# Performance work log

Hardware: AMD Instinct MI355X
Metric: run time of the kernel (lower is better)

## Reference

```python
import jax, jax.numpy as jnp
import numpy as np

HEADS = 8
DIM_HEAD = 64
QUERY_DIM = 320
INNER = HEADS * DIM_HEAD
B = 1
N = 2304          # 48*48 latent pixels
HS = WS = 48
SCALE = DIM_HEAD ** -0.5
ATTN_MATRIX_SCALE = 1.5   # injection_config['T']


def setup_inputs() -> dict:
    key = jax.random.key(0)
    ks = jax.random.split(key, 10)
    f = lambda k, s: jax.random.normal(k, s, dtype=jnp.float32)
    return {
        'x': f(ks[0], (B, N, QUERY_DIM)),
        'Wq': f(ks[1], (QUERY_DIM, INNER)) * 0.05,
        'Wo': f(ks[2], (INNER, QUERY_DIM)) * 0.05,
        'bo': jnp.zeros((QUERY_DIM,), jnp.float32),
        'q_injected': f(ks[3], (B * HEADS, N, DIM_HEAD)),
        'k_injected': f(ks[4], (B * HEADS, N, DIM_HEAD)),
        'v_injected': f(ks[5], (B * HEADS, N, DIM_HEAD)),
        'cnt_k_injected': f(ks[6], (B * HEADS, N, DIM_HEAD)),
        'cnt_v_injected': f(ks[7], (B * HEADS, N, DIM_HEAD)),
        'mask': jax.random.uniform(ks[8], (HS, WS), dtype=jnp.float32),
    }


def _split_heads(t):
    # 'b n (h d) -> (b h) n d'
    b, n, _ = t.shape
    return t.reshape(b, n, HEADS, DIM_HEAD).transpose(0, 2, 1, 3).reshape(b * HEADS, n, DIM_HEAD)


def reference(x, Wq, Wo, bo, q_injected, k_injected, v_injected,
              cnt_k_injected, cnt_v_injected, mask):
    # --- q/k/v with injection (b=1 so torch.cat([.]*b) is identity) ---
    q_in = q_injected                          # (bh, N, d)
    q_ = _split_heads(x @ Wq)                  # to_q(x) -> (bh, N, d)
    q = 0.5 * q_in + 0.5 * q_                  # blended query
    k = k_injected
    v = v_injected
    q_cnt, k_cnt, v_cnt = q_in, cnt_k_injected, cnt_v_injected

    # --- get_batch_sim: content-content similarity (b=1 => rearrange is identity) ---
    cc_sim = jnp.einsum('hid,hjd->hij', q_cnt, k_cnt) * SCALE     # (h, N, N)

    # --- get_batch_sim_with_mask ---
    sim = jnp.einsum('hid,hjd->hij', q, k) * (ATTN_MATRIX_SCALE * SCALE)  # (h, N, N)
    sim_r = sim.reshape(HEADS, HS, WS, N)
    cc_r = cc_sim.reshape(HEADS, HS, WS, N)
    max_sim = jnp.einsum('hid,hjd->hij', q_cnt, k)                # delta_q x delta_k (=self.k)
    max_sim_r = max_sim.reshape(HEADS, HS, WS, N)
    min_cc = jnp.min(cc_r, axis=3, keepdims=True)                 # (h, HS, WS, 1)
    max_ms = jnp.max(max_sim_r, axis=3, keepdims=True)            # (h, HS, WS, 1)

    # binary-threshold the mask, flip sign, bilinear-resize to (HS, WS)
    m = jnp.where(mask < 0.5, -1.0, jnp.where(mask > 0.5, 1.0, mask)) * -1.0
    m = jax.image.resize(m[None, None], (1, 1, HS, WS), method='bilinear')
    m = m.reshape(1, HS, WS, 1)

    gvm = (min_cc - max_ms) * m                                   # gradual_vanished_mask
    sim = (sim_r + gvm).reshape(HEADS, N, N)                      # rows [:WS] == all rows here

    # B=1 => the view/permute/reshape block is identity: sim, cc_sim are (h, N, N)
    # concatenated softmax over style keys and content keys
    cat_sim = jnp.concatenate([sim, cc_sim], axis=2)              # (h, N, 2N)
    cat_attn = jax.nn.softmax(cat_sim, axis=-1)
    cat_v = jnp.concatenate([v, v_cnt], axis=1)                   # (h, 2N, d)
    cat_out = jnp.einsum('hij,hjd->hid', cat_attn, cat_v)         # (h, N, d)

    # 'h (b n) d -> b n (h d)' with b=1
    out = cat_out.transpose(1, 0, 2).reshape(B, N, INNER)
    return out @ Wo + bo
```

## Files before the change

kernel.cpp:

```cpp
#include <hip/hip_runtime.h>
#include <math.h>

#define HEADS 8
#define NTOK  2304
#define DH    64
#define QD    320
#define INNER 512
#define TPS   36
#define PSTR  68

typedef _Float16 f16;
typedef f16  f16x4 __attribute__((ext_vector_type(4)));
typedef f16  f16x8 __attribute__((ext_vector_type(8)));
typedef float f32x4 __attribute__((ext_vector_type(4)));

#define MFMA(a,b,c) __builtin_amdgcn_mfma_f32_16x16x32_f16((a),(b),(c),0,0,0)

#define GLDS(gp, lp) __builtin_amdgcn_global_load_lds(                      \
    (const __attribute__((address_space(1))) void*)(gp),                    \
    (__attribute__((address_space(3))) void*)(lp), 16, 0, 0)

#if __has_builtin(__builtin_amdgcn_exp2f)
#define EXP2(x) __builtin_amdgcn_exp2f(x)
#else
#define EXP2(x) exp2f(x)
#endif

#define LOG2E 1.44269504f

static __device__ __forceinline__ unsigned pkrtz(float a, float b) {
#if __has_builtin(__builtin_amdgcn_cvt_pkrtz)
  return __builtin_bit_cast(unsigned, __builtin_amdgcn_cvt_pkrtz(a, b));
#else
  union { f16 h[2]; unsigned u; } c;
  c.h[0] = (f16)a; c.h[1] = (f16)b;
  return c.u;
#endif
}

__global__ __launch_bounds__(256) void prep_all(
    const float* __restrict__ qi, const float* __restrict__ ki,
    const float* __restrict__ kc, const float* __restrict__ x,
    const float* __restrict__ v,  const float* __restrict__ vc,
    const float* __restrict__ Wq, const float* __restrict__ Wo,
    f16* __restrict__ oq, f16* __restrict__ ok, f16* __restrict__ okc,
    f16* __restrict__ ox, f16* __restrict__ vt, f16* __restrict__ vct,
    f16* __restrict__ WqT, f16* __restrict__ WoT)
{
  __shared__ float T[64][65];
  const int bid = blockIdx.x;
  const int tid = threadIdx.x;

  if (bid < 2088) {
    int i = bid * 256 + tid;
    const float* src; f16* dst; float s = 1.0f; int off;
    if (i < 147456)      { src = qi; dst = oq;  off = i; }
    else if (i < 294912) { src = ki; dst = ok;  off = i - 147456; }
    else if (i < 442368) { src = kc; dst = okc; off = i - 294912; s = 0.125f * LOG2E; }
    else                 { src = x;  dst = ox;  off = i - 442368; }
    float4 a = reinterpret_cast<const float4*>(src)[off * 2];
    float4 b = reinterpret_cast<const float4*>(src)[off * 2 + 1];
    f16x8 o;
    o[0] = (f16)(a.x * s); o[1] = (f16)(a.y * s);
    o[2] = (f16)(a.z * s); o[3] = (f16)(a.w * s);
    o[4] = (f16)(b.x * s); o[5] = (f16)(b.y * s);
    o[6] = (f16)(b.z * s); o[7] = (f16)(b.w * s);
    *reinterpret_cast<f16x8*>(&dst[(size_t)off * 8]) = o;
  } else if (bid < 2664) {
    int t = bid - 2088;
    int z = t / 288, rem = t % 288;
    int h = rem / 36, nt = rem % 36;
    const float* src = z ? vc : v;
    f16* dst = z ? vct : vt;
    const int n0 = nt * 64;
    const size_t base = ((size_t)h * NTOK + n0) * DH;
    for (int it = 0; it < 4; ++it) {
      int idx = tid + it * 256;
      int n = idx >> 4, d0 = (idx & 15) * 4;
      float4 a = *reinterpret_cast<const float4*>(&src[base + (size_t)n * DH + d0]);
      T[n][d0] = a.x; T[n][d0 + 1] = a.y; T[n][d0 + 2] = a.z; T[n][d0 + 3] = a.w;
    }
    __syncthreads();
    for (int it = 0; it < 2; ++it) {
      int idx = tid + it * 256;
      int d = idx >> 3, c0 = (idx & 7) * 8;
      f16x8 o;
      #pragma unroll
      for (int i = 0; i < 8; ++i) o[i] = (f16)T[c0 + i][d];
      *reinterpret_cast<f16x8*>(&dst[(size_t)(h * 64 + d) * NTOK + n0 + c0]) = o;
    }
  } else {
    int t = bid - 2664;
    int z = t / 40, b = t % 40;
    const float* src = z ? Wo : Wq;
    f16* dst = z ? WoT : WqT;
    const int R = z ? INNER : QD;
    const int C = z ? QD : INNER;
    const int ctiles = C >> 6;
    const int rt = b / ctiles, ct = b % ctiles;
    for (int it = 0; it < 4; ++it) {
      int idx = tid + it * 256;
      int r = idx >> 4, c4 = (idx & 15) * 4;
      float4 a = *reinterpret_cast<const float4*>(&src[(size_t)(rt * 64 + r) * C + ct * 64 + c4]);
      T[r][c4] = a.x; T[r][c4 + 1] = a.y; T[r][c4 + 2] = a.z; T[r][c4 + 3] = a.w;
    }
    __syncthreads();
    for (int it = 0; it < 4; ++it) {
      int idx = tid + it * 256;
      int c = idx >> 4, r4 = (idx & 15) * 4;
      f16x4 o;
      #pragma unroll
      for (int i = 0; i < 4; ++i) o[i] = (f16)T[r4 + i][c];
      *reinterpret_cast<f16x4*>(&dst[(size_t)(ct * 64 + c) * R + rt * 64 + r4]) = o;
    }
  }
}

__global__ __launch_bounds__(256) void qblend_mfma(
    const f16* __restrict__ x16, const f16* __restrict__ WqT,
    const float* __restrict__ qinj, f16* __restrict__ qhat)
{
  const int qt = blockIdx.x, h = blockIdx.y;
  const int n0 = qt * 32;
  const int tid = threadIdx.x;
  const int w = tid >> 6, l = tid & 63, lq = l & 15, lk = l >> 4;
  const int qsub = w & 1, ch = w >> 1;
  f32x4 acc[2] = {};
  const f16* arow = x16 + (size_t)(n0 + qsub * 16 + lq) * QD;
  #pragma unroll
  for (int ks = 0; ks < 10; ++ks) {
    f16x8 a = *reinterpret_cast<const f16x8*>(&arow[ks * 32 + lk * 8]);
    #pragma unroll
    for (int df = 0; df < 2; ++df) {
      const f16* brow = WqT + (size_t)(h * 64 + ch * 32 + df * 16 + lq) * QD;
      f16x8 b = *reinterpret_cast<const f16x8*>(&brow[ks * 32 + lk * 8]);
      acc[df] = MFMA(a, b, acc[df]);
    }
  }
  const float sc = 0.09375f * LOG2E;
  #pragma unroll
  for (int df = 0; df < 2; ++df)
    #pragma unroll
    for (int r = 0; r < 4; ++r) {
      int n = n0 + qsub * 16 + lk * 4 + r;
      int d = ch * 32 + df * 16 + lq;
      size_t idx = ((size_t)h * NTOK + n) * DH + d;
      qhat[idx] = (f16)(sc * (qinj[idx] + acc[df][r]));
    }
}

__global__ __launch_bounds__(128, 2) void attn_nx(
    const f16* __restrict__ qhat, const f16* __restrict__ qc16,
    const f16* __restrict__ k16,  const f16* __restrict__ kc16,
    const f16* __restrict__ vt16, const f16* __restrict__ vct16,
    float* __restrict__ part)
{
  __shared__ __align__(16) f16 smem[2][2][2048];
  __shared__ __align__(16) f16 pbuf[2][640];

  const int bid = blockIdx.x;
  const int h    = bid & 7;
  const int strm = (bid >> 3) & 1;
  const int sp   = (bid >> 4) & 1;
  const int qt   = bid >> 5;
  const int tid = threadIdx.x;
  const int w = tid >> 6, l = tid & 63;
  const int lq = l & 15, lk = l >> 4;
  const size_t hb = (size_t)h * NTOK * DH;
  const int row0 = qt * 96 + w * 48 + lq;

  f16x8 qh0[2], qh1[2], qh2[2], qc0[2], qc1[2], qc2[2];
  {
    const size_t qr0 = hb + (size_t)row0 * DH;
    #pragma unroll
    for (int ks = 0; ks < 2; ++ks) {
      const int o = ks * 32 + lk * 8;
      qc0[ks] = *reinterpret_cast<const f16x8*>(&qc16[qr0 + o]);
      qc1[ks] = *reinterpret_cast<const f16x8*>(&qc16[qr0 + 16 * DH + o]);
      qc2[ks] = *reinterpret_cast<const f16x8*>(&qc16[qr0 + 32 * DH + o]);
      if (!strm) {
        qh0[ks] = *reinterpret_cast<const f16x8*>(&qhat[qr0 + o]);
        qh1[ks] = *reinterpret_cast<const f16x8*>(&qhat[qr0 + 16 * DH + o]);
        qh2[ks] = *reinterpret_cast<const f16x8*>(&qhat[qr0 + 32 * DH + o]);
      } else { qh0[ks] = qc0[ks]; qh1[ks] = qc1[ks]; qh2[ks] = qc2[ks]; }
    }
  }

  const int krow = tid >> 3;
  const int ksw  = ((tid & 7) ^ (krow & 7)) * 8;
  const int vrow = tid >> 2;
  const int voff = (tid & 3) * 8;
  const f16* gK = (strm ? kc16 : k16) + hb;
  const f16* gV = (strm ? vct16 : vt16) + (size_t)h * DH * NTOK;
  const int lb0 = __builtin_amdgcn_readfirstlane((tid & 64) * 8);
  const int lb1 = 1024 + lb0;

  #define STAGE(nb, j0)                                                      \
    do {                                                                     \
      GLDS(gK + (size_t)((j0) + krow) * 64 + ksw,        &smem[nb][0][lb0]); \
      GLDS(gK + (size_t)((j0) + 16 + krow) * 64 + ksw,   &smem[nb][0][lb1]); \
      GLDS(gV + (size_t)vrow * NTOK + (j0) + voff,       &smem[nb][1][lb0]); \
      GLDS(gV + (size_t)(32 + vrow) * NTOK + (j0) + voff,&smem[nb][1][lb1]); \
    } while (0)

  const int swz = (lq & 7) * 8;
  int xo[2];
  #pragma unroll
  for (int ks = 0; ks < 2; ++ks) xo[ks] = ((ks * 32 + lk * 8) ^ swz);

  float S0 = 0.f, S1 = 0.f, S2 = 0.f;
  float ax0, ax1, ax2;
  ax0 = ax1 = ax2 = strm ? INFINITY : -INFINITY;
  f32x4 O0[4] = {}, O1_[4] = {}, O2_[4] = {};
  f16* Pq = &pbuf[w][0];

  auto SMX = [&](const f32x4* s, float& Sl) -> f16x8 {
    float p0 = EXP2(s[0][0]), p1 = EXP2(s[0][1]);
    float p2 = EXP2(s[0][2]), p3 = EXP2(s[0][3]);
    float p4 = EXP2(s[1][0]), p5 = EXP2(s[1][1]);
    float p6 = EXP2(s[1][2]), p7 = EXP2(s[1][3]);
    Sl += ((p0 + p1) + (p2 + p3)) + ((p4 + p5) + (p6 + p7));
    uint2 wA, wB;
    wA.x = pkrtz(p0, p1); wA.y = pkrtz(p2, p3);
    wB.x = pkrtz(p4, p5); wB.y = pkrtz(p6, p7);
    *reinterpret_cast<uint2*>(Pq + lq * 40 + lk * 4)      = wA;
    *reinterpret_cast<uint2*>(Pq + lq * 40 + 16 + lk * 4) = wB;
    return *reinterpret_cast<const f16x8*>(Pq + lq * 40 + lk * 8);
  };

  const int jb = sp * (TPS * 32);
  STAGE(0, jb);
  asm volatile("s_waitcnt vmcnt(0)" ::: "memory");
  __builtin_amdgcn_sched_barrier(0);
  __builtin_amdgcn_s_barrier();
  __builtin_amdgcn_sched_barrier(0);

  int cur = 0;
  for (int t = 0; t < TPS; ++t) {
    if (t + 1 < TPS) STAGE(cur ^ 1, jb + (t + 1) * 32);

    const f16* Kb = &smem[cur][0][0];
    const f16* Vb = &smem[cur][1][0];

    f32x4 sA[2] = {}, sB[2] = {}, sC[2] = {};
    __builtin_amdgcn_s_setprio(1);
    if (!strm) {
      float m3A = -INFINITY, m3B = -INFINITY, m3C = -INFINITY;
      #pragma unroll
      for (int jf = 0; jf < 2; ++jf) {
        f32x4 tA = {}, tB = {}, tC = {};
        const int rb = (jf * 16 + lq) * 64;
        #pragma unroll
        for (int ks = 0; ks < 2; ++ks) {
          f16x8 aK = *reinterpret_cast<const f16x8*>(&Kb[rb + xo[ks]]);
          sA[jf] = MFMA(aK, qh0[ks], sA[jf]);
          sB[jf] = MFMA(aK, qh1[ks], sB[jf]);
          sC[jf] = MFMA(aK, qh2[ks], sC[jf]);
          tA = MFMA(aK, qc0[ks], tA);
          tB = MFMA(aK, qc1[ks], tB);
          tC = MFMA(aK, qc2[ks], tC);
        }
        m3A = fmaxf(m3A, fmaxf(fmaxf(tA[0], tA[1]), fmaxf(tA[2], tA[3])));
        m3B = fmaxf(m3B, fmaxf(fmaxf(tB[0], tB[1]), fmaxf(tB[2], tB[3])));
        m3C = fmaxf(m3C, fmaxf(fmaxf(tC[0], tC[1]), fmaxf(tC[2], tC[3])));
      }
      ax0 = fmaxf(ax0, m3A); ax1 = fmaxf(ax1, m3B); ax2 = fmaxf(ax2, m3C);
    } else {
      #pragma unroll
      for (int jf = 0; jf < 2; ++jf) {
        const int rb = (jf * 16 + lq) * 64;
        #pragma unroll
        for (int ks = 0; ks < 2; ++ks) {
          f16x8 aK = *reinterpret_cast<const f16x8*>(&Kb[rb + xo[ks]]);
          sA[jf] = MFMA(aK, qc0[ks], sA[jf]);
          sB[jf] = MFMA(aK, qc1[ks], sB[jf]);
          sC[jf] = MFMA(aK, qc2[ks], sC[jf]);
        }
      }
      ax0 = fminf(ax0, fminf(fminf(fminf(sA[0][0], sA[0][1]), fminf(sA[0][2], sA[0][3])),
                             fminf(fminf(sA[1][0], sA[1][1]), fminf(sA[1][2], sA[1][3]))));
      ax1 = fminf(ax1, fminf(fminf(fminf(sB[0][0], sB[0][1]), fminf(sB[0][2], sB[0][3])),
                             fminf(fminf(sB[1][0], sB[1][1]), fminf(sB[1][2], sB[1][3]))));
      ax2 = fminf(ax2, fminf(fminf(fminf(sC[0][0], sC[0][1]), fminf(sC[0][2], sC[0][3])),
                             fminf(fminf(sC[1][0], sC[1][1]), fminf(sC[1][2], sC[1][3]))));
    }
    __builtin_amdgcn_s_setprio(0);

    f16x8 pbA = SMX(sA, S0);
    f16x8 pbB = SMX(sB, S1);
    f16x8 pbC = SMX(sC, S2);

    __builtin_amdgcn_s_setprio(1);
    #pragma unroll
    for (int df = 0; df < 4; ++df) {
      f16x8 aV = *reinterpret_cast<const f16x8*>(&Vb[(df * 16 + lq) * 32 + lk * 8]);
      O0[df]  = MFMA(aV, pbA, O0[df]);
      O1_[df] = MFMA(aV, pbB, O1_[df]);
      O2_[df] = MFMA(aV, pbC, O2_[df]);
    }
    __builtin_amdgcn_s_setprio(0);

    asm volatile("s_waitcnt vmcnt(0)" ::: "memory");
    __builtin_amdgcn_sched_barrier(0);
    __builtin_amdgcn_s_barrier();
    __builtin_amdgcn_sched_barrier(0);
    cur ^= 1;
  }

  S0 += __shfl_xor(S0, 16); S0 += __shfl_xor(S0, 32);
  S1 += __shfl_xor(S1, 16); S1 += __shfl_xor(S1, 32);
  S2 += __shfl_xor(S2, 16); S2 += __shfl_xor(S2, 32);
  if (!strm) {
    ax0 = fmaxf(ax0, __shfl_xor(ax0, 16)); ax0 = fmaxf(ax0, __shfl_xor(ax0, 32));
    ax1 = fmaxf(ax1, __shfl_xor(ax1, 16)); ax1 = fmaxf(ax1, __shfl_xor(ax1, 32));
    ax2 = fmaxf(ax2, __shfl_xor(ax2, 16)); ax2 = fmaxf(ax2, __shfl_xor(ax2, 32));
  } else {
    ax0 = fminf(ax0, __shfl_xor(ax0, 16)); ax0 = fminf(ax0, __shfl_xor(ax0, 32));
    ax1 = fminf(ax1, __shfl_xor(ax1, 16)); ax1 = fminf(ax1, __shfl_xor(ax1, 32));
    ax2 = fminf(ax2, __shfl_xor(ax2, 16)); ax2 = fminf(ax2, __shfl_xor(ax2, 32));
  }
  {
    const size_t u = (size_t)((strm * 2 + sp) * 8 + h);
    float* p0 = part + (u * NTOK + (size_t)row0) * PSTR;
    float* p1 = p0 + (size_t)16 * PSTR;
    float* p2 = p0 + (size_t)32 * PSTR;
    #pragma unroll
    for (int df = 0; df < 4; ++df) {
      *reinterpret_cast<f32x4*>(p0 + df * 16 + lk * 4) = O0[df];
      *reinterpret_cast<f32x4*>(p1 + df * 16 + lk * 4) = O1_[df];
      *reinterpret_cast<f32x4*>(p2 + df * 16 + lk * 4) = O2_[df];
    }
    if (lk == 0) {
      p0[64] = S0; p0[65] = ax0;
      p1[64] = S1; p1[65] = ax1;
      p2[64] = S2; p2[65] = ax2;
    }
  }
  #undef STAGE
}

__global__ __launch_bounds__(256) void merge4(
    const float* __restrict__ part, const float* __restrict__ mask,
    f16* __restrict__ mid)
{
  const int qt = blockIdx.x, h = blockIdx.y;
  const int tid = threadIdx.x;
  const int r = tid >> 2, ds = (tid & 3) * 16;
  const int n = qt * 64 + r;
  const float* pA0 = part + ((size_t)(0  + h) * NTOK + n) * PSTR;
  const float* pA1 = part + ((size_t)(8  + h) * NTOK + n) * PSTR;
  const float* pB0 = part + ((size_t)(16 + h) * NTOK + n) * PSTR;
  const float* pB1 = part + ((size_t)(24 + h) * NTOK + n) * PSTR;

  float S1 = pA0[64] + pA1[64];
  float S2 = pB0[64] + pB1[64];
  float mx = fmaxf(pA0[65], pA1[65]);
  float mn = fminf(pB0[65], pB1[65]);

  float mv = mask[n];
  float mm = (mv < 0.5f) ? 1.0f : (mv > 0.5f ? -1.0f : -mv);
  float gvm = (mn - mx * LOG2E) * mm;
  float A1 = gvm;
  float Mf = fmaxf(A1, 0.0f);
  float w1 = exp2f(A1 - Mf), w2 = exp2f(-Mf);
  float inv = 1.0f / (w1 * S1 + w2 * S2);

  f16 ov[16];
  #pragma unroll
  for (int c = 0; c < 4; ++c) {
    float4 o1a = *reinterpret_cast<const float4*>(pA0 + ds + c * 4);
    float4 o1b = *reinterpret_cast<const float4*>(pA1 + ds + c * 4);
    float4 o2a = *reinterpret_cast<const float4*>(pB0 + ds + c * 4);
    float4 o2b = *reinterpret_cast<const float4*>(pB1 + ds + c * 4);
    ov[c*4+0] = (f16)((w1 * (o1a.x + o1b.x) + w2 * (o2a.x + o2b.x)) * inv);
    ov[c*4+1] = (f16)((w1 * (o1a.y + o1b.y) + w2 * (o2a.y + o2b.y)) * inv);
    ov[c*4+2] = (f16)((w1 * (o1a.z + o1b.z) + w2 * (o2a.z + o2b.z)) * inv);
    ov[c*4+3] = (f16)((w1 * (o1a.w + o1b.w) + w2 * (o2a.w + o2b.w)) * inv);
  }
  f16* dst = mid + (size_t)n * INNER + h * 64 + ds;
  *reinterpret_cast<f16x8*>(dst)     = *reinterpret_cast<f16x8*>(&ov[0]);
  *reinterpret_cast<f16x8*>(dst + 8) = *reinterpret_cast<f16x8*>(&ov[8]);
}

__global__ __launch_bounds__(64) void out_mfma(
    const f16* __restrict__ mid, const f16* __restrict__ WoT,
    const float* __restrict__ bo, float* __restrict__ out)
{
  const int n0 = blockIdx.x * 16;
  const int o0 = blockIdx.y * 64;
  const int l = threadIdx.x, lq = l & 15, lk = l >> 4;
  f32x4 acc[4] = {};
  const f16* arow = mid + (size_t)(n0 + lq) * INNER;
  #pragma unroll
  for (int ks = 0; ks < 16; ++ks) {
    f16x8 a = *reinterpret_cast<const f16x8*>(&arow[ks * 32 + lk * 8]);
    #pragma unroll
    for (int df = 0; df < 4; ++df) {
      f16x8 b = *reinterpret_cast<const f16x8*>(
          &WoT[(size_t)(o0 + df * 16 + lq) * INNER + ks * 32 + lk * 8]);
      acc[df] = MFMA(a, b, acc[df]);
    }
  }
  #pragma unroll
  for (int df = 0; df < 4; ++df) {
    float bb = bo[o0 + df * 16 + lq];
    #pragma unroll
    for (int r = 0; r < 4; ++r) {
      int n = n0 + lk * 4 + r;
      out[(size_t)n * QD + o0 + df * 16 + lq] = acc[df][r] + bb;
    }
  }
}

extern "C" void kernel_launch(void* const* d_in, const int* in_sizes, int n_in,
                              void* d_out, int out_size, void* d_ws, size_t ws_size,
                              hipStream_t stream) {
  const float* x    = (const float*)d_in[0];
  const float* Wq   = (const float*)d_in[1];
  const float* Wo   = (const float*)d_in[2];
  const float* bo   = (const float*)d_in[3];
  const float* qinj = (const float*)d_in[4];
  const float* kinj = (const float*)d_in[5];
  const float* vinj = (const float*)d_in[6];
  const float* kcnt = (const float*)d_in[7];
  const float* vcnt = (const float*)d_in[8];
  const float* mask = (const float*)d_in[9];
  float* out = (float*)d_out;

  const size_t T = (size_t)HEADS * NTOK * DH;
  f16* qhat = (f16*)d_ws;
  f16* qc16 = qhat + T;
  f16* k16  = qc16 + T;
  f16* kc16 = k16  + T;
  f16* vt16 = kc16 + T;
  f16* vct16= vt16 + T;
  f16* mid  = vct16 + T;
  f16* x16  = mid;
  f16* WqT  = mid + 737280;
  f16* WoT  = mid + T;
  float* part = (float*)(WoT + 163840);

  prep_all   <<<2744, 256, 0, stream>>>(qinj, kinj, kcnt, x, vinj, vcnt, Wq, Wo,
                                        qc16, k16, kc16, x16, vt16, vct16, WqT, WoT);
  qblend_mfma<<<dim3(72, 8), 256, 0, stream>>>(x16, WqT, qinj, qhat);
  attn_nx    <<<768, 128, 0, stream>>>(qhat, qc16, k16, kc16, vt16, vct16, part);
  merge4     <<<dim3(36, 8), 256, 0, stream>>>(part, mask, mid);
  out_mfma   <<<dim3(144, 5), 64, 0, stream>>>(mid, WoT, bo, out);
}
```

Measured before the change: 88.18 us.

## Make attention blocks single-wave with triple-buffered LDS staging and no block barriers

The attention kernel now runs one wave per block, 1536 blocks of 64 threads, so each wave loads its own K/V tiles instead of sharing them across two waves. Because the block is a single wave, the per-tile s_barrier is removed. A three-deep LDS ring with partial vmcnt waits keeps two tiles in flight while computing. This removes barrier stalls and deepens prefetch, but doubles global/L2 traffic for K and V per query row and raises LDS use per wave.

Result: slower. 96.37 us (+9.3%).

```diff
diff --git a/kernel.cpp b/kernel.cpp
--- a/kernel.cpp
+++ b/kernel.cpp
@@ -149,25 +149,24 @@
     }
 }
 
-__global__ __launch_bounds__(128, 2) void attn_nx(
+__global__ __launch_bounds__(64) void attn_pw(
     const f16* __restrict__ qhat, const f16* __restrict__ qc16,
     const f16* __restrict__ k16,  const f16* __restrict__ kc16,
     const f16* __restrict__ vt16, const f16* __restrict__ vct16,
     float* __restrict__ part)
 {
-  __shared__ __align__(16) f16 smem[2][2][2048];
-  __shared__ __align__(16) f16 pbuf[2][640];
+  __shared__ __align__(16) f16 smem[3][2][2048];
+  __shared__ __align__(16) f16 pbuf[640];
 
   const int bid = blockIdx.x;
   const int h    = bid & 7;
   const int strm = (bid >> 3) & 1;
   const int sp   = (bid >> 4) & 1;
-  const int qt   = bid >> 5;
-  const int tid = threadIdx.x;
-  const int w = tid >> 6, l = tid & 63;
+  const int wq   = bid >> 5;
+  const int l = threadIdx.x;
   const int lq = l & 15, lk = l >> 4;
   const size_t hb = (size_t)h * NTOK * DH;
-  const int row0 = qt * 96 + w * 48 + lq;
+  const int row0 = wq * 48 + lq;
 
   f16x8 qh0[2], qh1[2], qh2[2], qc0[2], qc1[2], qc2[2];
   {
@@ -186,21 +185,22 @@
     }
   }
 
-  const int krow = tid >> 3;
-  const int ksw  = ((tid & 7) ^ (krow & 7)) * 8;
-  const int vrow = tid >> 2;
-  const int voff = (tid & 3) * 8;
+  const int ksw  = ((l & 7) ^ (l >> 3)) * 8;
+  const int krw  = l >> 3;
+  const int vrw  = l >> 2;
+  const int voff = (l & 3) * 8;
   const f16* gK = (strm ? kc16 : k16) + hb;
   const f16* gV = (strm ? vct16 : vt16) + (size_t)h * DH * NTOK;
-  const int lb0 = __builtin_amdgcn_readfirstlane((tid & 64) * 8);
-  const int lb1 = 1024 + lb0;
-
-  #define STAGE(nb, j0)                                                      \
-    do {                                                                     \
-      GLDS(gK + (size_t)((j0) + krow) * 64 + ksw,        &smem[nb][0][lb0]); \
-      GLDS(gK + (size_t)((j0) + 16 + krow) * 64 + ksw,   &smem[nb][0][lb1]); \
-      GLDS(gV + (size_t)vrow * NTOK + (j0) + voff,       &smem[nb][1][lb0]); \
-      GLDS(gV + (size_t)(32 + vrow) * NTOK + (j0) + voff,&smem[nb][1][lb1]); \
+
+  #define STAGE(nb, j0)                                                       \
+    do {                                                                      \
+      _Pragma("unroll")                                                       \
+      for (int c = 0; c < 4; ++c) {                                           \
+        GLDS(gK + (size_t)((j0) + c * 8 + krw) * 64 + ksw,                    \
+             &smem[nb][0][c * 512]);                                          \
+        GLDS(gV + (size_t)(c * 16 + vrw) * NTOK + (j0) + voff,                \
+             &smem[nb][1][c * 512]);                                          \
+      }                                                                       \
     } while (0)
 
   const int swz = (lq & 7) * 8;
@@ -212,7 +212,6 @@
   float ax0, ax1, ax2;
   ax0 = ax1 = ax2 = strm ? INFINITY : -INFINITY;
   f32x4 O0[4] = {}, O1_[4] = {}, O2_[4] = {};
-  f16* Pq = &pbuf[w][0];
 
   auto SMX = [&](const f32x4* s, float& Sl) -> f16x8 {
     float p0 = EXP2(s[0][0]), p1 = EXP2(s[0][1]);
@@ -223,24 +222,29 @@
     uint2 wA, wB;
     wA.x = pkrtz(p0, p1); wA.y = pkrtz(p2, p3);
     wB.x = pkrtz(p4, p5); wB.y = pkrtz(p6, p7);
-    *reinterpret_cast<uint2*>(Pq + lq * 40 + lk * 4)      = wA;
-    *reinterpret_cast<uint2*>(Pq + lq * 40 + 16 + lk * 4) = wB;
-    return *reinterpret_cast<const f16x8*>(Pq + lq * 40 + lk * 8);
+    *reinterpret_cast<uint2*>(pbuf + lq * 40 + lk * 4)      = wA;
+    *reinterpret_cast<uint2*>(pbuf + lq * 40 + 16 + lk * 4) = wB;
+    return *reinterpret_cast<const f16x8*>(pbuf + lq * 40 + lk * 8);
   };
 
   const int jb = sp * (TPS * 32);
   STAGE(0, jb);
-  asm volatile("s_waitcnt vmcnt(0)" ::: "memory");
-  __builtin_amdgcn_sched_barrier(0);
-  __builtin_amdgcn_s_barrier();
-  __builtin_amdgcn_sched_barrier(0);
-
-  int cur = 0;
+  STAGE(1, jb + 32);
+
   for (int t = 0; t < TPS; ++t) {
-    if (t + 1 < TPS) STAGE(cur ^ 1, jb + (t + 1) * 32);
-
-    const f16* Kb = &smem[cur][0][0];
-    const f16* Vb = &smem[cur][1][0];
+    if (t + 2 < TPS) {
+      STAGE((t + 2) % 3, jb + (t + 2) * 32);
+      asm volatile("s_waitcnt vmcnt(16)" ::: "memory");
+    } else if (t + 1 < TPS) {
+      asm volatile("s_waitcnt vmcnt(8)" ::: "memory");
+    } else {
+      asm volatile("s_waitcnt vmcnt(0)" ::: "memory");
+    }
+    __builtin_amdgcn_sched_barrier(0);
+
+    const int bi = t % 3;
+    const f16* Kb = &smem[bi][0][0];
+    const f16* Vb = &smem[bi][1][0];
 
     f32x4 sA[2] = {}, sB[2] = {}, sC[2] = {};
     __builtin_amdgcn_s_setprio(1);
@@ -299,12 +303,6 @@
       O2_[df] = MFMA(aV, pbC, O2_[df]);
     }
     __builtin_amdgcn_s_setprio(0);
-
-    asm volatile("s_waitcnt vmcnt(0)" ::: "memory");
-    __builtin_amdgcn_sched_barrier(0);
-    __builtin_amdgcn_s_barrier();
-    __builtin_amdgcn_sched_barrier(0);
-    cur ^= 1;
   }
 
   S0 += __shfl_xor(S0, 16); S0 += __shfl_xor(S0, 32);
@@ -443,7 +441,7 @@
   prep_all   <<<2744, 256, 0, stream>>>(qinj, kinj, kcnt, x, vinj, vcnt, Wq, Wo,
                                         qc16, k16, kc16, x16, vt16, vct16, WqT, WoT);
   qblend_mfma<<<dim3(72, 8), 256, 0, stream>>>(x16, WqT, qinj, qhat);
-  attn_nx    <<<768, 128, 0, stream>>>(qhat, qc16, k16, kc16, vt16, vct16, part);
+  attn_pw    <<<1536, 64, 0, stream>>>(qhat, qc16, k16, kc16, vt16, vct16, part);
   merge4     <<<dim3(36, 8), 256, 0, stream>>>(part, mask, mid);
   out_mfma   <<<dim3(144, 5), 64, 0, stream>>>(mid, WoT, bo, out);
 }
```
